# Kernel optimization log

Hardware: AMD Instinct MI355X
Metric: run time of the kernel (lower is better)

Reference implementation:

```python
import jax, jax.numpy as jnp
import numpy as np

B, S, D, H, ROT = 2, 2048, 2048, 16, 64
HD = D // H  # 128


def setup_inputs() -> dict:
    key = jax.random.key(0)
    ks = jax.random.split(key, 6)
    sc = 0.02
    return {
        "hidden_states": jax.random.normal(ks[0], (B, S, D), jnp.float32),
        "attention_mask": jnp.zeros((B, 1, 1, S), jnp.float32),  # HF additive mask; 0 == keep
        "position_ids": jnp.tile(jnp.arange(S, dtype=jnp.int32), (B, 1)),
        "Wq": jax.random.normal(ks[1], (D, D), jnp.float32) * sc,
        "Wk": jax.random.normal(ks[2], (D, D), jnp.float32) * sc,
        "Wv": jax.random.normal(ks[3], (D, D), jnp.float32) * sc,
        "Wo": jax.random.normal(ks[4], (D, D), jnp.float32) * sc,
        "norm_const": 0.5 * jnp.ones((1, H, 1, 1), jnp.float32),
    }


def _rotate_every_two(x):
    x1 = x[..., ::2]
    x2 = x[..., 1::2]
    return jnp.stack((-x2, x1), axis=-1).reshape(x.shape)


def _apply_rope(x, sin, cos):
    # x: [B,S,H,ROT]; sin/cos: [B,S,ROT//2] -> repeat_interleave(2) as in GPT-J
    sin2 = jnp.repeat(sin, 2, axis=-1)[:, :, None, :]
    cos2 = jnp.repeat(cos, 2, axis=-1)[:, :, None, :]
    return x * cos2 + _rotate_every_two(x) * sin2


def reference(hidden_states, attention_mask, position_ids, Wq, Wk, Wv, Wo, norm_const):
    # projections (nn.Linear, no bias): y = x @ W^T
    q = (hidden_states @ Wq.T).reshape(B, S, H, HD)
    k = (hidden_states @ Wk.T).reshape(B, S, H, HD)
    v = (hidden_states @ Wv.T).reshape(B, S, H, HD).transpose(0, 2, 1, 3)  # [B,H,S,HD]

    # GPT-J sinusoidal rotary on first ROT dims
    inv_freq = 1.0 / (10000.0 ** (jnp.arange(0, ROT, 2, dtype=jnp.float32) / ROT))
    ang = position_ids.astype(jnp.float32)[:, :, None] * inv_freq  # [B,S,ROT//2]
    sin, cos = jnp.sin(ang), jnp.cos(ang)
    q = jnp.concatenate([_apply_rope(q[..., :ROT], sin, cos), q[..., ROT:]], axis=-1)
    k = jnp.concatenate([_apply_rope(k[..., :ROT], sin, cos), k[..., ROT:]], axis=-1)
    q = q.transpose(0, 2, 1, 3)  # [B,H,S,HD]
    k = k.transpose(0, 2, 1, 3)

    # cosine attention: L2-normalize q and k (F.normalize, eps=1e-12)
    eps = 1e-12
    qn = q / jnp.clip(jnp.linalg.norm(q, axis=-1, keepdims=True), eps)
    kn = k / jnp.clip(jnp.linalg.norm(k, axis=-1, keepdims=True), eps)

    keep = attention_mask == 0                               # [B,1,1,S] bool
    causal = jnp.tril(jnp.ones((S, S), bool))[None, None]    # [1,1,S,S]
    # per-query count of visible keys -> value rescale with learned exponent
    counts = jnp.sum((causal & keep).astype(jnp.float32), axis=-1, keepdims=True)  # [B,1,S,1]
    expo = jax.nn.sigmoid(norm_const)                        # [1,H,1,1]
    v = v / jnp.clip(counts ** expo, 1.0)                    # [B,H,S,HD]

    keep_t = jnp.swapaxes(keep, -1, -2).astype(q.dtype)      # [B,1,S,1]
    qn = qn * keep_t
    kn = kn * keep_t
    v = v * keep_t

    attn = jnp.einsum('bhqd,bhkd->bhqk', qn, kn)             # cosine scores
    attn = jnp.where(causal, attn, 0.0)                      # causal zero-mask (no softmax)
    out = jnp.einsum('bhqk,bhkd->bhqd', attn, v)             # [B,H,S,HD]
    out = out.transpose(0, 2, 1, 3).reshape(B, S, D)
    return out @ Wo.T
```

## Files before the change

kernel.cpp:

```cpp
#include <hip/hip_runtime.h>
#include <hip/hip_bf16.h>

typedef __attribute__((ext_vector_type(8))) short bf16x8;
typedef __attribute__((ext_vector_type(4))) float f32x4;
typedef unsigned short u16;
typedef unsigned int u32;

constexpr int B = 2, S = 2048, D = 2048, H = 16, HD = 128, ROT = 64;
constexpr int NQKV = 3 * D;

__device__ __forceinline__ void gload16(const u16* g, u16* l)
{
    __builtin_amdgcn_global_load_lds((const __attribute__((address_space(1))) void*)g,
                                     (__attribute__((address_space(3))) void*)l, 16, 0, 0);
}

__device__ __forceinline__ float bf2f(u32 lo16) { return __uint_as_float(lo16 << 16); }

__global__ void cast_kernel(const float* __restrict__ in, u16* __restrict__ out, int n4)
{
    int idx = blockIdx.x * blockDim.x + threadIdx.x;
    int stride = gridDim.x * blockDim.x;
    for (int i = idx; i < n4; i += stride) {
        float4 v = ((const float4*)in)[i];
        __hip_bfloat16 a = __float2bfloat16(v.x);
        __hip_bfloat16 b = __float2bfloat16(v.y);
        __hip_bfloat16 c = __float2bfloat16(v.z);
        __hip_bfloat16 d = __float2bfloat16(v.w);
        ushort4 o;
        o.x = *(u16*)&a; o.y = *(u16*)&b; o.z = *(u16*)&c; o.w = *(u16*)&d;
        ((ushort4*)out)[i] = o;
    }
}

__global__ void castw_kernel(const float* __restrict__ w0, const float* __restrict__ w1,
                             const float* __restrict__ w2, const float* __restrict__ w3,
                             u16* __restrict__ o0, u16* __restrict__ o1,
                             u16* __restrict__ o2, u16* __restrict__ o3, int n4)
{
    int which = blockIdx.y;
    const float* src = which == 0 ? w0 : which == 1 ? w1 : which == 2 ? w2 : w3;
    u16* dst = which == 0 ? o0 : which == 1 ? o1 : which == 2 ? o2 : o3;
    int idx = blockIdx.x * blockDim.x + threadIdx.x;
    int stride = gridDim.x * blockDim.x;
    for (int i = idx; i < n4; i += stride) {
        float4 v = ((const float4*)src)[i];
        __hip_bfloat16 a = __float2bfloat16(v.x);
        __hip_bfloat16 b = __float2bfloat16(v.y);
        __hip_bfloat16 c = __float2bfloat16(v.z);
        __hip_bfloat16 d = __float2bfloat16(v.w);
        ushort4 o;
        o.x = *(u16*)&a; o.y = *(u16*)&b; o.z = *(u16*)&c; o.w = *(u16*)&d;
        ((ushort4*)dst)[i] = o;
    }
}

__global__ void prep_kernel(const float* __restrict__ mask, const int* __restrict__ pos,
                            const float* __restrict__ ncst,
                            float* __restrict__ sinb, float* __restrict__ cosb,
                            float* __restrict__ keep, float* __restrict__ expo)
{
    int gid = blockIdx.x * blockDim.x + threadIdx.x;
    int total = B * S * 32;
    if (gid < total) {
        int j = gid & 31;
        int bs = gid >> 5;
        float p = (float)pos[bs];
        float f = powf(10000.f, -(float)j / 32.f);
        float ang = p * f;
        sinb[gid] = sinf(ang);
        cosb[gid] = cosf(ang);
        if (j == 0) keep[bs] = (mask[bs] == 0.f) ? 1.f : 0.f;
    }
    if (gid < H) expo[gid] = 1.f / (1.f + expf(-ncst[gid]));
}

__global__ void counts_kernel(const float* __restrict__ keep, float* __restrict__ counts)
{
    __shared__ float part[256];
    int b = blockIdx.x, t = threadIdx.x;
    float v[8];
    float s = 0.f;
    const float* kp = keep + b * S + t * 8;
#pragma unroll
    for (int i = 0; i < 8; ++i) { s += kp[i]; v[i] = s; }
    part[t] = s;
    __syncthreads();
    float off = 0.f;
    for (int j = 0; j < t; ++j) off += part[j];
    float* cp = counts + b * S + t * 8;
#pragma unroll
    for (int i = 0; i < 8; ++i) cp[i] = off + v[i];
}


template <int CNT>
__device__ __forceinline__ void stage_op(const u16* __restrict__ G, int K,
                                         int trow0, int kt, u16* lbuf, int tid)
{
#pragma unroll
    for (int l = 0; l < CNT; ++l) {
        int idx = l * 512 + tid;
        int row = idx >> 2;
        int slot = idx & 3;
        int col8 = slot ^ ((row >> 1) & 3);
        const u16* g = G + (size_t)(trow0 + row) * K + kt * 32 + col8 * 8;
        u16* ld = lbuf + (size_t)(idx & ~63) * 8;
        gload16(g, ld);
    }
}

template <int BM, int BN, int CA, int CB, int MR, int NR, int BF16OUT>
__global__ __launch_bounds__(512, 2) void gemm32(
    const u16* __restrict__ A, const u16* __restrict__ Bm,
    float* __restrict__ Cf, u16* __restrict__ Cb, int N, int K, int ntn)
{
    __shared__ u16 As[2 * BM * 32];
    __shared__ u16 Bs[2 * BN * 32];
    const int tid = threadIdx.x;
    const int lane = tid & 63;
    const int w = tid >> 6;
    const int wm = w >> 2;
    const int wn = w & 3;
    const int l15 = lane & 15, l4 = lane >> 4;

    int nwg = gridDim.x;
    int bid = blockIdx.x;
    int cpx = nwg >> 3;
    int sbid = (bid & 7) * cpx + (bid >> 3);
    int bm = sbid / ntn, bn = sbid % ntn;
    const int bmrow = bm * BM, bnrow = bn * BN;

    f32x4 acc[MR][NR] = {};
    const int nk = K >> 5;

    stage_op<CA>(A, K, bmrow, 0, &As[0], tid);
    stage_op<CB>(Bm, K, bnrow, 0, &Bs[0], tid);

    for (int t = 0; t < nk; ++t) {
        const u16* ab = &As[(t & 1) * BM * 32];
        const u16* bb = &Bs[(t & 1) * BN * 32];
        if (t + 1 < nk) {
            stage_op<CA>(A, K, bmrow, t + 1, &As[((t + 1) & 1) * BM * 32], tid);
            stage_op<CB>(Bm, K, bnrow, t + 1, &Bs[((t + 1) & 1) * BN * 32], tid);
            asm volatile("s_waitcnt vmcnt(%0)" :: "i"(CA + CB) : "memory");
        } else {
            asm volatile("s_waitcnt vmcnt(0)" ::: "memory");
        }
        __builtin_amdgcn_sched_barrier(0);
        __builtin_amdgcn_s_barrier();

        bf16x8 af[MR];
#pragma unroll
        for (int i = 0; i < MR; ++i) {
            int row = wm * (BM / 2) + i * 16 + l15;
            int slot = l4 ^ ((row >> 1) & 3);
            af[i] = *(const bf16x8*)(ab + row * 32 + slot * 8);
        }
#pragma unroll
        for (int n = 0; n < NR; ++n) {
            int brow = wn * (BN / 4) + n * 16 + l15;
            int bslot = l4 ^ ((brow >> 1) & 3);
            bf16x8 bf = *(const bf16x8*)(bb + brow * 32 + bslot * 8);
            __builtin_amdgcn_s_setprio(1);
#pragma unroll
            for (int i = 0; i < MR; ++i)
                acc[i][n] = __builtin_amdgcn_mfma_f32_16x16x32_bf16(af[i], bf, acc[i][n], 0, 0, 0);
            __builtin_amdgcn_s_setprio(0);
        }
        __builtin_amdgcn_sched_barrier(0);
        __builtin_amdgcn_s_barrier();
    }

#pragma unroll
    for (int i = 0; i < MR; ++i) {
        int row = bmrow + wm * (BM / 2) + i * 16 + l4 * 4;
#pragma unroll
        for (int n = 0; n < NR; ++n) {
            int col = bnrow + wn * (BN / 4) + n * 16 + l15;
            f32x4 v = acc[i][n];
#pragma unroll
            for (int r = 0; r < 4; ++r) {
                if (BF16OUT) {
                    __hip_bfloat16 hv = __float2bfloat16(v[r]);
                    Cb[(size_t)(row + r) * N + col] = *(u16*)&hv;
                } else {
                    Cf[(size_t)(row + r) * N + col] = v[r];
                }
            }
        }
    }
}

__global__ void postproc_all(const u16* __restrict__ tmpb,
                             u16* __restrict__ qn, u16* __restrict__ kn, u16* __restrict__ vT,
                             const float* __restrict__ sinb, const float* __restrict__ cosb,
                             const float* __restrict__ keep, const float* __restrict__ counts,
                             const float* __restrict__ expo)
{
    int gw = (blockIdx.x * blockDim.x + threadIdx.x) >> 6;
    int lane = threadIdx.x & 63;
    if (gw >= B * S * H) return;
    int h = gw % H;
    int sb = gw / H;
    int s = sb % S;
    int b = sb / S;
    const u16* rowp = tmpb + (size_t)(b * S + s) * NQKV;
    u32 qv = *(const u32*)(rowp + h * 128 + lane * 2);
    u32 kv = *(const u32*)(rowp + D + h * 128 + lane * 2);
    u32 vv = *(const u32*)(rowp + 2 * D + h * 128 + lane * 2);
    float q0 = bf2f(qv & 0xffff), q1 = bf2f(qv >> 16);
    float k0 = bf2f(kv & 0xffff), k1 = bf2f(kv >> 16);
    float v0 = bf2f(vv & 0xffff), v1 = bf2f(vv >> 16);
    if (lane < 32) {
        float sn = sinb[(b * S + s) * 32 + lane];
        float cs = cosb[(b * S + s) * 32 + lane];
        float nq0 = q0 * cs - q1 * sn, nq1 = q1 * cs + q0 * sn;
        float nk0 = k0 * cs - k1 * sn, nk1 = k1 * cs + k0 * sn;
        q0 = nq0; q1 = nq1; k0 = nk0; k1 = nk1;
    }
    float sq = q0 * q0 + q1 * q1;
    float sk = k0 * k0 + k1 * k1;
#pragma unroll
    for (int o = 1; o < 64; o <<= 1) {
        sq += __shfl_xor(sq, o, 64);
        sk += __shfl_xor(sk, o, 64);
    }
    float kf = keep[b * S + s];
    float scq = kf / fmaxf(sqrtf(sq), 1e-12f);
    float sck = kf / fmaxf(sqrtf(sk), 1e-12f);
    float cnt = counts[b * S + s];
    float e = expo[h];
    float scv = kf / fmaxf(powf(cnt, e), 1.0f);

    __hip_bfloat16 a0 = __float2bfloat16(q0 * scq), a1 = __float2bfloat16(q1 * scq);
    __hip_bfloat16 b0 = __float2bfloat16(k0 * sck), b1 = __float2bfloat16(k1 * sck);
    __hip_bfloat16 c0 = __float2bfloat16(v0 * scv), c1 = __float2bfloat16(v1 * scv);
    size_t obase = ((size_t)(b * H + h) * S + s) * 128 + lane * 2;
    *(u32*)(qn + obase) = (u32)*(u16*)&a0 | ((u32)*(u16*)&a1 << 16);
    *(u32*)(kn + obase) = (u32)*(u16*)&b0 | ((u32)*(u16*)&b1 << 16);
    size_t vbase = ((size_t)(b * H + h) * 128) * (size_t)S + s;
    vT[vbase + (size_t)(2 * lane) * S] = *(u16*)&c0;
    vT[vbase + (size_t)(2 * lane + 1) * S] = *(u16*)&c1;
}

__global__ __launch_bounds__(256) void chunk_state(
    const u16* __restrict__ kn, const u16* __restrict__ vT, u16* __restrict__ T16)
{
    __shared__ u16 As[128][72];
    __shared__ u16 Bs[128][72];
    int tid = threadIdx.x, lane = tid & 63, w = tid >> 6;
    int wm = w >> 1, wn = w & 1;
    int c = blockIdx.x, bh = blockIdx.y;
    const int l15 = lane & 15, l4 = lane >> 4;
    size_t vbase = (size_t)bh * 128 * S;
    size_t kbase = (size_t)bh * S * 128;
    f32x4 acc[4][4] = {};

    for (int t = 0; t < 2; ++t) {
#pragma unroll
        for (int i = 0; i < 4; ++i) {
            int q = tid + i * 256;
            int r = q >> 3, c8 = q & 7;
            uint4 v = *(const uint4*)(vT + vbase + (size_t)r * S + c * 128 + t * 64 + c8 * 8);
            *(uint4*)(&As[r][c8 * 8]) = v;
        }
#pragma unroll
        for (int i = 0; i < 4; ++i) {
            int q = tid + i * 256;
            int r = q >> 4, c16 = q & 15;
            uint4 v = *(const uint4*)(kn + kbase + (size_t)(c * 128 + t * 64 + r) * 128 + c16 * 8);
            const u16* pv = (const u16*)&v;
#pragma unroll
            for (int j = 0; j < 8; ++j) Bs[c16 * 8 + j][r] = pv[j];
        }
        __syncthreads();
#pragma unroll
        for (int tt = 0; tt < 2; ++tt) {
            bf16x8 a[4], b[4];
#pragma unroll
            for (int m = 0; m < 4; ++m)
                a[m] = *(const bf16x8*)(&As[wm * 64 + m * 16 + l15][tt * 32 + l4 * 8]);
#pragma unroll
            for (int n = 0; n < 4; ++n)
                b[n] = *(const bf16x8*)(&Bs[wn * 64 + n * 16 + l15][tt * 32 + l4 * 8]);
#pragma unroll
            for (int m = 0; m < 4; ++m)
#pragma unroll
                for (int n = 0; n < 4; ++n)
                    acc[m][n] = __builtin_amdgcn_mfma_f32_16x16x32_bf16(a[m], b[n], acc[m][n], 0, 0, 0);
        }
        __syncthreads();
    }
#pragma unroll
    for (int m = 0; m < 4; ++m) {
        int row = wm * 64 + m * 16 + l4 * 4;
#pragma unroll
        for (int n = 0; n < 4; ++n) {
            int col = wn * 64 + n * 16 + l15;
#pragma unroll
            for (int r = 0; r < 4; ++r) {
                __hip_bfloat16 hv = __float2bfloat16(acc[m][n][r]);
                T16[((size_t)(bh * 16 + c) * 128 + row + r) * 128 + col] = *(u16*)&hv;
            }
        }
    }
}

__global__ void prefix_state(const u16* __restrict__ T16, u16* __restrict__ P16)
{
    int g = blockIdx.x * blockDim.x + threadIdx.x;
    int bh = g >> 11;
    int i8 = (g & 2047) * 8;
    const u16* tp = T16 + (size_t)bh * 16 * 16384 + i8;
    u16* pp = P16 + (size_t)bh * 16 * 16384 + i8;
    float run[8] = {};
    for (int c = 0; c < 16; ++c) {
        u16 ob[8];
#pragma unroll
        for (int j = 0; j < 8; ++j) { __hip_bfloat16 hv = __float2bfloat16(run[j]); ob[j] = *(u16*)&hv; }
        *(uint4*)(pp + (size_t)c * 16384) = *(uint4*)ob;
        uint4 tv = *(const uint4*)(tp + (size_t)c * 16384);
        const u16* tvp = (const u16*)&tv;
#pragma unroll
        for (int j = 0; j < 8; ++j) run[j] += bf2f(tvp[j]);
    }
}

__global__ __launch_bounds__(256, 2) void attn2(
    const u16* __restrict__ qn, const u16* __restrict__ kn,
    const u16* __restrict__ vT, const u16* __restrict__ P16, u16* __restrict__ ao)
{
    __shared__ u16 KN[64][136];
    __shared__ u16 VT[128][72];
    __shared__ u16 SC[128][72];
    int tid = threadIdx.x, lane = tid & 63, w = tid >> 6;
    int c = blockIdx.x, bh = blockIdx.y;
    int b = bh >> 4, h = bh & 15;
    const int l15 = lane & 15, l4 = lane >> 4;
    size_t base = (size_t)bh * S * 128;
    size_t vbase = (size_t)bh * 128 * S;
    const u16* Pp = P16 + (size_t)(bh * 16 + c) * 16384;

    bf16x8 qa[2][4];
#pragma unroll
    for (int m = 0; m < 2; ++m)
#pragma unroll
        for (int t = 0; t < 4; ++t) {
            int row = c * 128 + w * 32 + m * 16 + l15;
            qa[m][t] = *(const bf16x8*)(qn + base + (size_t)row * 128 + t * 32 + l4 * 8);
        }

    f32x4 acc[2][8] = {};

#pragma unroll
    for (int pt = 0; pt < 2; ++pt) {
#pragma unroll
        for (int i = 0; i < 4; ++i) {
            int q = tid + i * 256;
            int r = q >> 3, c8 = q & 7;
            uint4 v = *(const uint4*)(Pp + (size_t)r * 128 + pt * 64 + c8 * 8);
            *(uint4*)(&VT[r][c8 * 8]) = v;
        }
        __syncthreads();
#pragma unroll
        for (int tt = 0; tt < 2; ++tt) {
            bf16x8 pb[8];
#pragma unroll
            for (int n = 0; n < 8; ++n)
                pb[n] = *(const bf16x8*)(&VT[n * 16 + l15][tt * 32 + l4 * 8]);
#pragma unroll
            for (int m = 0; m < 2; ++m)
#pragma unroll
                for (int n = 0; n < 8; ++n)
                    acc[m][n] = __builtin_amdgcn_mfma_f32_16x16x32_bf16(qa[m][pt * 2 + tt], pb[n], acc[m][n], 0, 0, 0);
        }
        __syncthreads();
    }

    for (int kt2 = 0; kt2 < 2; ++kt2) {
#pragma unroll
        for (int i = 0; i < 4; ++i) {
            int q = tid + i * 256;
            int r = q >> 4, c8 = q & 15;
            uint4 v = *(const uint4*)(kn + base + (size_t)(c * 128 + kt2 * 64 + r) * 128 + c8 * 8);
            *(uint4*)(&KN[r][c8 * 8]) = v;
        }
#pragma unroll
        for (int i = 0; i < 4; ++i) {
            int q = tid + i * 256;
            int r = q >> 3, c8 = q & 7;
            uint4 v = *(const uint4*)(vT + vbase + (size_t)r * S + c * 128 + kt2 * 64 + c8 * 8);
            *(uint4*)(&VT[r][c8 * 8]) = v;
        }
        __syncthreads();
        f32x4 sacc[2][4] = {};
#pragma unroll
        for (int t = 0; t < 4; ++t) {
            bf16x8 kb[4];
#pragma unroll
            for (int n = 0; n < 4; ++n)
                kb[n] = *(const bf16x8*)(&KN[n * 16 + l15][t * 32 + l4 * 8]);
#pragma unroll
            for (int m = 0; m < 2; ++m)
#pragma unroll
                for (int n = 0; n < 4; ++n)
                    sacc[m][n] = __builtin_amdgcn_mfma_f32_16x16x32_bf16(qa[m][t], kb[n], sacc[m][n], 0, 0, 0);
        }
#pragma unroll
        for (int m = 0; m < 2; ++m)
#pragma unroll
            for (int n = 0; n < 4; ++n)
#pragma unroll
                for (int r = 0; r < 4; ++r) {
                    int rowl = w * 32 + m * 16 + l4 * 4 + r;
                    int coll = n * 16 + l15;
                    int kl = kt2 * 64 + coll;
                    float val = (kl <= rowl) ? sacc[m][n][r] : 0.f;
                    __hip_bfloat16 hv = __float2bfloat16(val);
                    SC[rowl][coll] = *(u16*)&hv;
                }
#pragma unroll
        for (int t = 0; t < 2; ++t) {
            bf16x8 sa[2], vb[8];
#pragma unroll
            for (int m = 0; m < 2; ++m)
                sa[m] = *(const bf16x8*)(&SC[w * 32 + m * 16 + l15][t * 32 + l4 * 8]);
#pragma unroll
            for (int n = 0; n < 8; ++n)
                vb[n] = *(const bf16x8*)(&VT[n * 16 + l15][t * 32 + l4 * 8]);
#pragma unroll
            for (int m = 0; m < 2; ++m)
#pragma unroll
                for (int n = 0; n < 8; ++n)
                    acc[m][n] = __builtin_amdgcn_mfma_f32_16x16x32_bf16(sa[m], vb[n], acc[m][n], 0, 0, 0);
        }
        __syncthreads();
    }

#pragma unroll
    for (int m = 0; m < 2; ++m)
#pragma unroll
        for (int n = 0; n < 8; ++n)
#pragma unroll
            for (int r = 0; r < 4; ++r) {
                int srow = c * 128 + w * 32 + m * 16 + l4 * 4 + r;
                int d = n * 16 + l15;
                __hip_bfloat16 hv = __float2bfloat16(acc[m][n][r]);
                ao[(size_t)(b * S + srow) * D + h * 128 + d] = *(u16*)&hv;
            }
}

extern "C" void kernel_launch(void* const* d_in, const int* in_sizes, int n_in,
                              void* d_out, int out_size, void* d_ws, size_t ws_size,
                              hipStream_t stream)
{
    const float* hs = (const float*)d_in[0];
    const float* mask = (const float*)d_in[1];
    const int* pos = (const int*)d_in[2];
    const float* Wq = (const float*)d_in[3];
    const float* Wk = (const float*)d_in[4];
    const float* Wv = (const float*)d_in[5];
    const float* Wo = (const float*)d_in[6];
    const float* ncst = (const float*)d_in[7];
    float* out = (float*)d_out;

    char* ws = (char*)d_ws;
    size_t off = 0;
    auto alloc = [&](size_t bytes) {
        size_t o = off;
        off += (bytes + 255) & ~(size_t)255;
        return o;
    };
    u16* hs16 = (u16*)(ws + alloc((size_t)B * S * D * 2));
    u16* wqkv16 = (u16*)(ws + alloc((size_t)NQKV * D * 2));
    u16* wo16 = (u16*)(ws + alloc((size_t)D * D * 2));
    u16* tmpb = (u16*)(ws + alloc((size_t)B * S * NQKV * 2));
    u16* qn16 = (u16*)(ws + alloc((size_t)B * S * D * 2));
    u16* kn16 = (u16*)(ws + alloc((size_t)B * S * D * 2));
    u16* vT16 = (u16*)(ws + alloc((size_t)B * S * D * 2));
    float* sinb = (float*)(ws + alloc((size_t)B * S * 32 * 4));
    float* cosb = (float*)(ws + alloc((size_t)B * S * 32 * 4));
    float* keep = (float*)(ws + alloc((size_t)B * S * 4));
    float* counts = (float*)(ws + alloc((size_t)B * S * 4));
    float* expo = (float*)(ws + alloc(64));
    u16* ao16 = tmpb;
    u16* T16 = tmpb + (size_t)8388608;
    u16* P16 = tmpb + (size_t)16777216;

    cast_kernel<<<2048, 256, 0, stream>>>(hs, hs16, B * S * D / 4);
    castw_kernel<<<dim3(512, 4), 256, 0, stream>>>(
        Wq, Wk, Wv, Wo,
        wqkv16, wqkv16 + (size_t)D * D, wqkv16 + (size_t)2 * D * D, wo16, D * D / 4);
    prep_kernel<<<(B * S * 32 + 255) / 256, 256, 0, stream>>>(mask, pos, ncst, sinb, cosb, keep, expo);
    counts_kernel<<<B, 256, 0, stream>>>(keep, counts);

    gemm32<256, 384, 2, 3, 8, 6, 1><<<256, 512, 0, stream>>>(
        hs16, wqkv16, nullptr, tmpb, NQKV, D, NQKV / 384);

    postproc_all<<<(B * S * H) / 4, 256, 0, stream>>>(tmpb, qn16, kn16, vT16, sinb, cosb, keep, counts, expo);

    dim3 gc(S / 128, B * H);
    chunk_state<<<gc, 256, 0, stream>>>(kn16, vT16, T16);
    prefix_state<<<256, 256, 0, stream>>>(T16, P16);
    attn2<<<gc, 256, 0, stream>>>(qn16, kn16, vT16, P16, ao16);

    gemm32<128, 256, 1, 2, 4, 4, 0><<<256, 512, 0, stream>>>(
        ao16, wo16, out, nullptr, D, D, D / 256);
}
```

Before: 288.1 us.

## Triple-buffer GEMM staging and store V row-major instead of transposed

The GEMM main loop moves from double to triple-buffered LDS staging, prefetching two k-tiles ahead so global loads get more time to overlap MFMA work. Separately, postproc now writes V row-major with coalesced 32-bit stores instead of strided scalar transposed stores. chunk_state and attn2 transpose V while copying it into LDS. This raises GEMM LDS use, which may threaten 2-blocks-per-CU occupancy for the large 256x384 tile, and adds scattered 16-bit LDS writes in the attention kernels.

```diff
diff --git a/kernel.cpp b/kernel.cpp
--- a/kernel.cpp
+++ b/kernel.cpp
@@ -115,8 +115,8 @@
     const u16* __restrict__ A, const u16* __restrict__ Bm,
     float* __restrict__ Cf, u16* __restrict__ Cb, int N, int K, int ntn)
 {
-    __shared__ u16 As[2 * BM * 32];
-    __shared__ u16 Bs[2 * BN * 32];
+    __shared__ u16 As[3 * BM * 32];
+    __shared__ u16 Bs[3 * BN * 32];
     const int tid = threadIdx.x;
     const int lane = tid & 63;
     const int w = tid >> 6;
@@ -136,13 +136,19 @@
 
     stage_op<CA>(A, K, bmrow, 0, &As[0], tid);
     stage_op<CB>(Bm, K, bnrow, 0, &Bs[0], tid);
-
+    stage_op<CA>(A, K, bmrow, 1, &As[BM * 32], tid);
+    stage_op<CB>(Bm, K, bnrow, 1, &Bs[BN * 32], tid);
+
+    int c0 = 0;
     for (int t = 0; t < nk; ++t) {
-        const u16* ab = &As[(t & 1) * BM * 32];
-        const u16* bb = &Bs[(t & 1) * BN * 32];
-        if (t + 1 < nk) {
-            stage_op<CA>(A, K, bmrow, t + 1, &As[((t + 1) & 1) * BM * 32], tid);
-            stage_op<CB>(Bm, K, bnrow, t + 1, &Bs[((t + 1) & 1) * BN * 32], tid);
+        const u16* ab = &As[c0 * BM * 32];
+        const u16* bb = &Bs[c0 * BN * 32];
+        if (t + 2 < nk) {
+            int c2 = c0 + 2; if (c2 >= 3) c2 -= 3;
+            stage_op<CA>(A, K, bmrow, t + 2, &As[c2 * BM * 32], tid);
+            stage_op<CB>(Bm, K, bnrow, t + 2, &Bs[c2 * BN * 32], tid);
+            asm volatile("s_waitcnt vmcnt(%0)" :: "i"(2 * (CA + CB)) : "memory");
+        } else if (t + 1 < nk) {
             asm volatile("s_waitcnt vmcnt(%0)" :: "i"(CA + CB) : "memory");
         } else {
             asm volatile("s_waitcnt vmcnt(0)" ::: "memory");
@@ -170,6 +176,7 @@
         }
         __builtin_amdgcn_sched_barrier(0);
         __builtin_amdgcn_s_barrier();
+        c0 = (c0 + 1 == 3) ? 0 : c0 + 1;
     }
 
 #pragma unroll
@@ -193,7 +200,7 @@
 }
 
 __global__ void postproc_all(const u16* __restrict__ tmpb,
-                             u16* __restrict__ qn, u16* __restrict__ kn, u16* __restrict__ vT,
+                             u16* __restrict__ qn, u16* __restrict__ kn, u16* __restrict__ vr,
                              const float* __restrict__ sinb, const float* __restrict__ cosb,
                              const float* __restrict__ keep, const float* __restrict__ counts,
                              const float* __restrict__ expo)
@@ -239,13 +246,11 @@
     size_t obase = ((size_t)(b * H + h) * S + s) * 128 + lane * 2;
     *(u32*)(qn + obase) = (u32)*(u16*)&a0 | ((u32)*(u16*)&a1 << 16);
     *(u32*)(kn + obase) = (u32)*(u16*)&b0 | ((u32)*(u16*)&b1 << 16);
-    size_t vbase = ((size_t)(b * H + h) * 128) * (size_t)S + s;
-    vT[vbase + (size_t)(2 * lane) * S] = *(u16*)&c0;
-    vT[vbase + (size_t)(2 * lane + 1) * S] = *(u16*)&c1;
+    *(u32*)(vr + obase) = (u32)*(u16*)&c0 | ((u32)*(u16*)&c1 << 16);
 }
 
 __global__ __launch_bounds__(256) void chunk_state(
-    const u16* __restrict__ kn, const u16* __restrict__ vT, u16* __restrict__ T16)
+    const u16* __restrict__ kn, const u16* __restrict__ vr, u16* __restrict__ T16)
 {
     __shared__ u16 As[128][72];
     __shared__ u16 Bs[128][72];
@@ -253,23 +258,24 @@
     int wm = w >> 1, wn = w & 1;
     int c = blockIdx.x, bh = blockIdx.y;
     const int l15 = lane & 15, l4 = lane >> 4;
-    size_t vbase = (size_t)bh * 128 * S;
-    size_t kbase = (size_t)bh * S * 128;
+    size_t base = (size_t)bh * S * 128;
     f32x4 acc[4][4] = {};
 
     for (int t = 0; t < 2; ++t) {
-#pragma unroll
-        for (int i = 0; i < 4; ++i) {
-            int q = tid + i * 256;
-            int r = q >> 3, c8 = q & 7;
-            uint4 v = *(const uint4*)(vT + vbase + (size_t)r * S + c * 128 + t * 64 + c8 * 8);
-            *(uint4*)(&As[r][c8 * 8]) = v;
-        }
 #pragma unroll
         for (int i = 0; i < 4; ++i) {
             int q = tid + i * 256;
             int r = q >> 4, c16 = q & 15;
-            uint4 v = *(const uint4*)(kn + kbase + (size_t)(c * 128 + t * 64 + r) * 128 + c16 * 8);
+            uint4 v = *(const uint4*)(vr + base + (size_t)(c * 128 + t * 64 + r) * 128 + c16 * 8);
+            const u16* pv = (const u16*)&v;
+#pragma unroll
+            for (int j = 0; j < 8; ++j) As[c16 * 8 + j][r] = pv[j];
+        }
+#pragma unroll
+        for (int i = 0; i < 4; ++i) {
+            int q = tid + i * 256;
+            int r = q >> 4, c16 = q & 15;
+            uint4 v = *(const uint4*)(kn + base + (size_t)(c * 128 + t * 64 + r) * 128 + c16 * 8);
             const u16* pv = (const u16*)&v;
 #pragma unroll
             for (int j = 0; j < 8; ++j) Bs[c16 * 8 + j][r] = pv[j];
@@ -329,7 +335,7 @@
 
 __global__ __launch_bounds__(256, 2) void attn2(
     const u16* __restrict__ qn, const u16* __restrict__ kn,
-    const u16* __restrict__ vT, const u16* __restrict__ P16, u16* __restrict__ ao)
+    const u16* __restrict__ vr, const u16* __restrict__ P16, u16* __restrict__ ao)
 {
     __shared__ u16 KN[64][136];
     __shared__ u16 VT[128][72];
@@ -339,7 +345,6 @@
     int b = bh >> 4, h = bh & 15;
     const int l15 = lane & 15, l4 = lane >> 4;
     size_t base = (size_t)bh * S * 128;
-    size_t vbase = (size_t)bh * 128 * S;
     const u16* Pp = P16 + (size_t)(bh * 16 + c) * 16384;
 
     bf16x8 qa[2][4];
@@ -389,9 +394,11 @@
 #pragma unroll
         for (int i = 0; i < 4; ++i) {
             int q = tid + i * 256;
-            int r = q >> 3, c8 = q & 7;
-            uint4 v = *(const uint4*)(vT + vbase + (size_t)r * S + c * 128 + kt2 * 64 + c8 * 8);
-            *(uint4*)(&VT[r][c8 * 8]) = v;
+            int r = q >> 4, c16 = q & 15;
+            uint4 v = *(const uint4*)(vr + base + (size_t)(c * 128 + kt2 * 64 + r) * 128 + c16 * 8);
+            const u16* pv = (const u16*)&v;
+#pragma unroll
+            for (int j = 0; j < 8; ++j) VT[c16 * 8 + j][r] = pv[j];
         }
         __syncthreads();
         f32x4 sacc[2][4] = {};
@@ -478,7 +485,7 @@
     u16* tmpb = (u16*)(ws + alloc((size_t)B * S * NQKV * 2));
     u16* qn16 = (u16*)(ws + alloc((size_t)B * S * D * 2));
     u16* kn16 = (u16*)(ws + alloc((size_t)B * S * D * 2));
-    u16* vT16 = (u16*)(ws + alloc((size_t)B * S * D * 2));
+    u16* vr16 = (u16*)(ws + alloc((size_t)B * S * D * 2));
     float* sinb = (float*)(ws + alloc((size_t)B * S * 32 * 4));
     float* cosb = (float*)(ws + alloc((size_t)B * S * 32 * 4));
     float* keep = (float*)(ws + alloc((size_t)B * S * 4));
@@ -498,12 +505,12 @@
     gemm32<256, 384, 2, 3, 8, 6, 1><<<256, 512, 0, stream>>>(
         hs16, wqkv16, nullptr, tmpb, NQKV, D, NQKV / 384);
 
-    postproc_all<<<(B * S * H) / 4, 256, 0, stream>>>(tmpb, qn16, kn16, vT16, sinb, cosb, keep, counts, expo);
+    postproc_all<<<(B * S * H) / 4, 256, 0, stream>>>(tmpb, qn16, kn16, vr16, sinb, cosb, keep, counts, expo);
 
     dim3 gc(S / 128, B * H);
-    chunk_state<<<gc, 256, 0, stream>>>(kn16, vT16, T16);
+    chunk_state<<<gc, 256, 0, stream>>>(kn16, vr16, T16);
     prefix_state<<<256, 256, 0, stream>>>(T16, P16);
-    attn2<<<gc, 256, 0, stream>>>(qn16, kn16, vT16, P16, ao16);
+    attn2<<<gc, 256, 0, stream>>>(qn16, kn16, vr16, P16, ao16);
 
     gemm32<128, 256, 1, 2, 4, 4, 0><<<256, 512, 0, stream>>>(
         ao16, wo16, out, nullptr, D, D, D / 256);
```

After: 282.8 us. Within noise of the previous version (-1.9%).
